# Kernel optimization log

Measured on AMD Instinct MI355X. Metric: run time of the kernel, lower is better.

## Reference

```python
import jax, jax.numpy as jnp
import numpy as np
from math import sqrt

B, S, E, H = 2, 2048, 768, 12
DH = E // H
W = 256            # one-sided attention window (attention_window=512)
G = 16             # number of global tokens (positions 0..G-1 in every batch row)
PAD = 128          # last PAD tokens per row are padding (masked)
FF = 3072          # SwiGLU intermediate size
NEG = -1e9
EPS = 1e-5


def _ln(x, g, b):
    m = jnp.mean(x, axis=-1, keepdims=True)
    v = jnp.var(x, axis=-1, keepdims=True)
    return (x - m) * jax.lax.rsqrt(v + EPS) * g + b


def _rope(x, t):
    # x: [B,H,S,DH]; t: [B,S] float 'set positions'
    half = DH // 2
    inv_freq = 1.0 / (10000.0 ** (jnp.arange(half, dtype=jnp.float32) / half))
    ang = t[:, None, :, None] * inv_freq            # [B,1,S,half]
    cos, sin = jnp.cos(ang), jnp.sin(ang)
    x1, x2 = x[..., :half], x[..., half:]
    return jnp.concatenate([x1 * cos - x2 * sin, x2 * cos + x1 * sin], axis=-1)


def _heads(x):  # [B,S,E] -> [B,H,S,DH]
    return x.reshape(B, S, H, DH).transpose(0, 2, 1, 3)


def _chunk3(x):
    # [B,H,S,D] -> [B,H,C,3W,D]: for query chunk c, keys from chunks c-1,c,c+1 (zero padded)
    b, h, s, d = x.shape
    c = s // W
    xp = jnp.pad(x, ((0, 0), (0, 0), (W, W), (0, 0))).reshape(b, h, c + 2, W, d)
    return jnp.concatenate([xp[:, :, :-2], xp[:, :, 1:-1], xp[:, :, 2:]], axis=3)


def _forward(x, attention_mask, global_attention_mask,
             Wq, bq, Wk, bk, Wv, bv, Wqg, bqg, Wkg, bkg, Wvg, bvg,
             ln0_g, ln0_b, ln1_g, ln1_b, W1, W3, W2):
    C = S // W
    merged = attention_mask * (global_attention_mask + 1)   # 0 masked, 1 local, 2 global
    is_masked = merged == 0
    is_global = merged == 2
    remove = merged != 1   # keys removed from windowed attention (masked or global)

    q = _heads(x @ Wq + bq) / sqrt(DH)
    k = _heads(x @ Wk + bk)
    v = _heads(x @ Wv + bv)

    # RoPE over 'set positions': (~is_index_masked) * cumsum(is_index_global_attn)
    t = jnp.where(is_masked, 0, jnp.cumsum(is_global.astype(jnp.int32), axis=1)).astype(jnp.float32)
    q = _rope(q, t)
    k = _rope(k, t)

    # --- sliding-window (banded) scores: band[b,h,i,d] = q_i . k_{i+d-W} ---
    qc = q.reshape(B, H, C, W, DH)
    k3 = _chunk3(k)
    s3 = jnp.einsum('bhcpd,bhcqd->bhcpq', qc, k3)                     # [B,H,C,W,3W]
    didx = jnp.arange(W)[:, None] + jnp.arange(2 * W + 1)[None, :]    # [W,2W+1]
    band = jnp.take_along_axis(s3, didx[None, None, None], axis=-1)   # [B,H,C,W,2W+1]

    # mask removed keys / out-of-range positions inside the band
    rmp = jnp.pad(remove, ((0, 0), (W, W)), constant_values=True).reshape(B, C + 2, W)
    rm3 = jnp.concatenate([rmp[:, :-2], rmp[:, 1:-1], rmp[:, 2:]], axis=2)  # [B,C,3W]
    band_rm = jnp.take_along_axis(jnp.broadcast_to(rm3[:, :, None, :], (B, C, W, 3 * W)),
                                  didx[None, None], axis=-1)                # [B,C,W,2W+1]
    band = jnp.where(band_rm[:, None], NEG, band).reshape(B, H, S, 2 * W + 1)

    # --- global-key columns (keys taken from the RoPE'd local key vectors) ---
    sg = jnp.einsum('bhid,bhgd->bhig', q, k[:, :, :G])                # [B,H,S,G]

    scores = jnp.concatenate([sg, band], axis=-1)                     # [B,H,S,G+2W+1]
    probs = jax.nn.softmax(scores.astype(jnp.float32), axis=-1).astype(x.dtype)
    probs = jnp.where(is_masked[:, None, :, None], 0.0, probs)

    # --- probs @ value: global columns + band ---
    out = jnp.einsum('bhig,bhgd->bhid', probs[..., :G], v[:, :, :G])
    pl = probs[..., G:].reshape(B, H, C, W, 2 * W + 1)
    rows = jnp.broadcast_to(jnp.arange(W)[:, None], (W, 2 * W + 1))
    p3 = jnp.zeros((B, H, C, W, 3 * W), probs.dtype).at[:, :, :, rows, didx].set(pl)
    v3 = _chunk3(v)
    out = out + jnp.einsum('bhcpq,bhcqd->bhcpd', p3, v3).reshape(B, H, S, DH)
    attn = out.transpose(0, 2, 1, 3).reshape(B, S, E)

    # --- full attention for global tokens (separate global projections, no RoPE) ---
    gq = _heads(x @ Wqg + bqg)[:, :, :G] / sqrt(DH)                   # [B,H,G,DH]
    gk = _heads(x @ Wkg + bkg)
    gv = _heads(x @ Wvg + bvg)
    gs = jnp.einsum('bhgd,bhjd->bhgj', gq, gk)                        # [B,H,G,S]
    gs = jnp.where(is_masked[:, None, None, :], NEG, gs)
    gp = jax.nn.softmax(gs.astype(jnp.float32), axis=-1).astype(x.dtype)
    gout = jnp.einsum('bhgj,bhjd->bhgd', gp, gv).transpose(0, 2, 1, 3).reshape(B, G, E)
    attn = attn.at[:, :G].set(gout)

    # residual + post-LN, SwiGLU FFN, residual + post-LN (dropout = eval mode)
    h0 = _ln(x + attn, ln0_g, ln0_b)
    ffn = (jax.nn.silu(h0 @ W1) * (h0 @ W3)) @ W2
    return _ln(h0 + ffn, ln1_g, ln1_b)


def setup_inputs():
    key = jax.random.key(0)
    ks = jax.random.split(key, 12)
    x = jax.random.normal(ks[0], (B, S, E), jnp.float32)
    attention_mask = jnp.ones((B, S), jnp.int32).at[:, S - PAD:].set(0)
    global_attention_mask = jnp.zeros((B, S), jnp.int32).at[:, :G].set(1)
    sd = 0.02
    def w(k, shape):
        return jax.random.normal(k, shape, jnp.float32) * sd
    return dict(
        x=x, attention_mask=attention_mask, global_attention_mask=global_attention_mask,
        Wq=w(ks[1], (E, E)), bq=jnp.zeros((E,), jnp.float32),
        Wk=w(ks[2], (E, E)), bk=jnp.zeros((E,), jnp.float32),
        Wv=w(ks[3], (E, E)), bv=jnp.zeros((E,), jnp.float32),
        Wqg=w(ks[4], (E, E)), bqg=jnp.zeros((E,), jnp.float32),
        Wkg=w(ks[5], (E, E)), bkg=jnp.zeros((E,), jnp.float32),
        Wvg=w(ks[6], (E, E)), bvg=jnp.zeros((E,), jnp.float32),
        ln0_g=jnp.ones((E,), jnp.float32), ln0_b=jnp.zeros((E,), jnp.float32),
        ln1_g=jnp.ones((E,), jnp.float32), ln1_b=jnp.zeros((E,), jnp.float32),
        W1=w(ks[7], (E, FF)), W3=w(ks[8], (E, FF)), W2=w(ks[9], (FF, E)))


def reference(x, attention_mask, global_attention_mask, Wq, bq, Wk, bk, Wv, bv,
              Wqg, bqg, Wkg, bkg, Wvg, bvg, ln0_g, ln0_b, ln1_g, ln1_b, W1, W3, W2):
    return _forward(x, attention_mask, global_attention_mask,
                    Wq, bq, Wk, bk, Wv, bv, Wqg, bqg, Wkg, bkg, Wvg, bvg,
                    ln0_g, ln0_b, ln1_g, ln1_b, W1, W3, W2)
```

## Files before the change

kernel.cpp:

```cpp
#include <hip/hip_runtime.h>


#define BB_ 2
#define SS 2048
#define EE 768
#define HH 12
#define DHH 64
#define GG 16
#define FFN 3072
#define MM (BB_*SS)

typedef __bf16 bf16_t;
typedef __bf16 bf16x8_t __attribute__((ext_vector_type(8)));
typedef float f32x4_t __attribute__((ext_vector_type(4)));

__device__ inline void gload16(const void* g, void* l) {
  __builtin_amdgcn_global_load_lds((const __attribute__((address_space(1))) void*)g,
                                   (__attribute__((address_space(3))) void*)l, 16, 0, 0);
}

__global__ __launch_bounds__(64) void detect_kernel(const unsigned int* __restrict__ w,
                                                    int* __restrict__ flag) {
  int cnt = 0;
  for (int i = threadIdx.x; i < 1024; i += 64) {
    unsigned e = (w[i] >> 7) & 0xFF;
    cnt += (e >= 100 && e <= 144) ? 1 : 0;
  }
  for (int off = 32; off; off >>= 1) cnt += __shfl_xor(cnt, off);
  if (threadIdx.x == 0) flag[0] = (cnt > 512) ? 1 : 0;
}

struct CanonP { const void* src[11]; bf16_t* dst[11]; };

__global__ __launch_bounds__(256) void canon_kernel(CanonP P, const int* __restrict__ flag) {
  constexpr int ns[11] = {3145728, 768,768,768,768,768,768, 768,768,768,768};
  int idx4 = (blockIdx.x*256 + threadIdx.x)*4;
  const bool isb = flag[0] != 0;
  int off = 0, seg = -1, loc = 0;
  #pragma unroll
  for (int i=0;i<11;i++) {
    if (seg < 0 && idx4 < off + ns[i]) { seg = i; loc = idx4 - off; }
    off += ns[i];
  }
  if (seg < 0) return;
  const void* s = P.src[seg];
  bf16_t* d = P.dst[seg];
  if (isb) {
    *(uint2*)&d[loc] = *(const uint2*)((const unsigned short*)s + loc);
  } else {
    float4 v = *(const float4*)((const float*)s + loc);
    d[loc+0] = (bf16_t)v.x; d[loc+1] = (bf16_t)v.y;
    d[loc+2] = (bf16_t)v.z; d[loc+3] = (bf16_t)v.w;
  }
}

struct TP6 { const void* s[6]; bf16_t* d[6]; };

__global__ __launch_bounds__(256) void trans_kernel(TP6 P, int R, int C,
                                                    const int* __restrict__ flag) {
  const int z = blockIdx.z;
  const void* src = P.s[z]; bf16_t* dst = P.d[z];
  const bool isb = flag[0] != 0;
  __shared__ bf16_t tile[32][33];
  int tx = threadIdx.x & 31, ty = threadIdx.x >> 5;
  int r0 = blockIdx.y*32, c0 = blockIdx.x*32;
  #pragma unroll
  for (int i=0;i<4;i++) {
    int rr = ty + i*8;
    size_t si = (size_t)(r0+rr)*C + c0 + tx;
    tile[rr][tx] = isb ? ((const bf16_t*)src)[si] : (bf16_t)((const float*)src)[si];
  }
  __syncthreads();
  #pragma unroll
  for (int i=0;i<4;i++) {
    int cc = ty + i*8;
    dst[(size_t)(c0+cc)*R + r0 + tx] = tile[tx][cc];
  }
}

__global__ __launch_bounds__(256) void zero_kernel(float* __restrict__ p, int n) {
  int i = blockIdx.x*256 + threadIdx.x;
  if (i < n) p[i] = 0.f;
}

__global__ __launch_bounds__(256) void flags_kernel(const int* __restrict__ am,
                                                    const int* __restrict__ gm,
                                                    float* __restrict__ tpos,
                                                    int* __restrict__ flags) {
  int b = blockIdx.x;
  int t = threadIdx.x;
  int lane = t & 63, wv = t >> 6;
  int base = b*SS + t*8;
  int mg[8]; int isg[8]; int loc = 0;
  for (int i=0;i<8;i++) {
    int a = am[base+i], g = gm[base+i];
    int merged = a*(g+1);
    mg[i] = merged;
    isg[i] = (merged==2) ? 1 : 0;
    loc += isg[i];
  }
  int x = loc;
  for (int off=1; off<64; off<<=1) {
    int y = __shfl_up(x, off);
    if (lane >= off) x += y;
  }
  __shared__ int wtot[4];
  if (lane==63) wtot[wv] = x;
  __syncthreads();
  int prev = 0;
  for (int w=0; w<wv; w++) prev += wtot[w];
  int run = prev + x - loc;
  for (int i=0;i<8;i++) {
    run += isg[i];
    int masked = (mg[i]==0) ? 1 : 0;
    int glob   = (mg[i]==2) ? 1 : 0;
    int rem    = (mg[i]!=1) ? 1 : 0;
    tpos[base+i]  = masked ? 0.f : (float)run;
    flags[base+i] = masked | (glob<<1) | (rem<<2);
  }
}

__device__ inline void gemm128_core(const bf16_t* __restrict__ A,
                                    const bf16_t* __restrict__ BT,
                                    int ldA, int ldB, int kbeg, int kend,
                                    int m0, int n0,
                                    bf16_t* As, bf16_t* Bs,
                                    f32x4_t (&acc)[4][4]) {
  const int t = threadIdx.x;
  const int lane = t & 63, wv = t >> 6;
  const int l15 = lane & 15, quad = lane >> 4;
  const int wr = (wv >> 1) << 6, wc = (wv & 1) << 6;
  const int rsub = lane >> 3, pch = lane & 7;
  const int sch = pch ^ rsub;
  const size_t abase = (size_t)(m0 + wv*32 + rsub)*ldA + sch*8;
  const size_t bbase = (size_t)(n0 + wv*32 + rsub)*ldB + sch*8;
  const int sx = l15 & 7;
  bf16_t* lA = As + (wv*32)*64;
  bf16_t* lB = Bs + (wv*32)*64;
  for (int k0 = kbeg; k0 < kend; k0 += 64) {
    __syncthreads();
    #pragma unroll
    for (int j=0;j<4;j++) {
      gload16(A + abase + (size_t)(j*8)*ldA + k0, lA + j*8*64);
      gload16(BT + bbase + (size_t)(j*8)*ldB + k0, lB + j*8*64);
    }
    __syncthreads();
    #pragma unroll
    for (int c=0;c<2;c++) {
      bf16x8_t af[4], bfr[4];
      #pragma unroll
      for (int a=0;a<4;a++)
        af[a] = *(const bf16x8_t*)&As[(wr + a*16 + l15)*64 + ((c*4+quad)^sx)*8];
      #pragma unroll
      for (int b=0;b<4;b++)
        bfr[b] = *(const bf16x8_t*)&Bs[(wc + b*16 + l15)*64 + ((c*4+quad)^sx)*8];
      #pragma unroll
      for (int a=0;a<4;a++)
        #pragma unroll
        for (int b=0;b<4;b++)
          acc[a][b] = __builtin_amdgcn_mfma_f32_16x16x32_bf16(af[a], bfr[b], acc[a][b], 0,0,0);
    }
  }
}

struct ProjParams {
  const bf16_t* W[5];
  const bf16_t* Bi[5];
  bf16_t* O[5];
};

__global__ __launch_bounds__(256) void proj_kernel(const bf16_t* __restrict__ x,
                                                   ProjParams P,
                                                   const float* __restrict__ tpos) {
  const int m0 = blockIdx.x*128, n0 = blockIdx.y*128;
  const int z  = blockIdx.z;
  __shared__ bf16_t As[128*64];
  __shared__ bf16_t Bs[128*64];
  f32x4_t acc[4][4];
  #pragma unroll
  for (int a=0;a<4;a++)
    #pragma unroll
    for (int b=0;b<4;b++) acc[a][b] = (f32x4_t){0.f,0.f,0.f,0.f};
  gemm128_core(x, P.W[z], EE, EE, 0, EE, m0, n0, As, Bs, acc);

  const int t = threadIdx.x;
  const int lane = t & 63, wv = t >> 6;
  const int l15 = lane & 15, quad = lane >> 4;
  const int wr = (wv >> 1) << 6, wc = (wv & 1) << 6;
  const float scale = (z==0) ? 0.125f : 1.f;
  const bool rope = (z<2);
  const int h = (n0 + wc) >> 6;
  bf16_t* Oz = P.O[z];
  const bf16_t* Bz = P.Bi[z];
  float bvals[4];
  #pragma unroll
  for (int b=0;b<4;b++) bvals[b] = (float)Bz[h*64 + b*16 + l15];
  #pragma unroll
  for (int a=0;a<4;a++) {
    #pragma unroll
    for (int r=0;r<4;r++) {
      int row = m0 + wr + a*16 + quad*4 + r;
      int bb = row >> 11, spos = row & (SS-1);
      float vals[4];
      #pragma unroll
      for (int b=0;b<4;b++) vals[b] = (acc[a][b][r] + bvals[b]) * scale;
      if (rope) {
        float tv = tpos[row];
        #pragma unroll
        for (int b=0;b<2;b++) {
          int j = b*16 + l15;
          float inv = __expf(-(float)j * (9.210340371976184f/32.f));
          float ang = tv * inv;
          float sn = __sinf(ang), cs = __cosf(ang);
          float x1 = vals[b], x2 = vals[b+2];
          vals[b]   = x1*cs - x2*sn;
          vals[b+2] = x2*cs + x1*sn;
        }
      }
      bf16_t* dst = Oz + ((size_t)(bb*HH + h)*SS + spos)*DHH;
      #pragma unroll
      for (int b=0;b<4;b++) dst[b*16 + l15] = (bf16_t)vals[b];
    }
  }
}

__global__ __launch_bounds__(256) void gemm_ffn13(const bf16_t* __restrict__ A,
                                                  const bf16_t* __restrict__ B1T,
                                                  const bf16_t* __restrict__ B3T,
                                                  bf16_t* __restrict__ g1) {
  const int m0 = blockIdx.x*128, n0 = blockIdx.y*128;
  const int t = threadIdx.x;
  const int lane = t & 63, wv = t >> 6;
  const int l15 = lane & 15, quad = lane >> 4;
  const int wr = (wv >> 1) << 6, wc = (wv & 1) << 6;
  const int rsub = lane >> 3, pch = lane & 7;
  const int sch = pch ^ rsub;
  const int sx = l15 & 7;
  __shared__ bf16_t As[128*64];
  __shared__ bf16_t B1s[128*64];
  __shared__ bf16_t B3s[128*64];
  f32x4_t acc1[4][4], acc3[4][4];
  #pragma unroll
  for (int a=0;a<4;a++)
    #pragma unroll
    for (int b=0;b<4;b++) {
      acc1[a][b] = (f32x4_t){0.f,0.f,0.f,0.f};
      acc3[a][b] = (f32x4_t){0.f,0.f,0.f,0.f};
    }
  const size_t abase = (size_t)(m0 + wv*32 + rsub)*EE + sch*8;
  const size_t bbase = (size_t)(n0 + wv*32 + rsub)*EE + sch*8;
  bf16_t* lA  = As  + (wv*32)*64;
  bf16_t* lB1 = B1s + (wv*32)*64;
  bf16_t* lB3 = B3s + (wv*32)*64;
  for (int k0 = 0; k0 < EE; k0 += 64) {
    __syncthreads();
    #pragma unroll
    for (int j=0;j<4;j++) {
      gload16(A   + abase + (size_t)(j*8)*EE + k0, lA  + j*8*64);
      gload16(B1T + bbase + (size_t)(j*8)*EE + k0, lB1 + j*8*64);
      gload16(B3T + bbase + (size_t)(j*8)*EE + k0, lB3 + j*8*64);
    }
    __syncthreads();
    #pragma unroll
    for (int c=0;c<2;c++) {
      bf16x8_t af[4], b1f[4], b3f[4];
      #pragma unroll
      for (int a=0;a<4;a++)
        af[a] = *(const bf16x8_t*)&As[(wr + a*16 + l15)*64 + ((c*4+quad)^sx)*8];
      #pragma unroll
      for (int b=0;b<4;b++) {
        b1f[b] = *(const bf16x8_t*)&B1s[(wc + b*16 + l15)*64 + ((c*4+quad)^sx)*8];
        b3f[b] = *(const bf16x8_t*)&B3s[(wc + b*16 + l15)*64 + ((c*4+quad)^sx)*8];
      }
      #pragma unroll
      for (int a=0;a<4;a++)
        #pragma unroll
        for (int b=0;b<4;b++) {
          acc1[a][b] = __builtin_amdgcn_mfma_f32_16x16x32_bf16(af[a], b1f[b], acc1[a][b], 0,0,0);
          acc3[a][b] = __builtin_amdgcn_mfma_f32_16x16x32_bf16(af[a], b3f[b], acc3[a][b], 0,0,0);
        }
    }
  }
  #pragma unroll
  for (int a=0;a<4;a++)
    #pragma unroll
    for (int r=0;r<4;r++) {
      int row = m0 + wr + a*16 + quad*4 + r;
      #pragma unroll
      for (int b=0;b<4;b++) {
        float a1 = acc1[a][b][r];
        float sil = a1 / (1.f + __expf(-a1));
        g1[(size_t)row*FFN + n0 + wc + b*16 + l15] = (bf16_t)(sil * acc3[a][b][r]);
      }
    }
}

struct Ffn2Out { float* p[4]; };

__global__ __launch_bounds__(256) void gemm_ffn2(const bf16_t* __restrict__ A,
                                                 const bf16_t* __restrict__ BT,
                                                 Ffn2Out O) {
  const int m0 = blockIdx.x*128, n0 = blockIdx.y*128;
  const int kz = blockIdx.z;
  __shared__ bf16_t As[128*64];
  __shared__ bf16_t Bs[128*64];
  f32x4_t acc[4][4];
  #pragma unroll
  for (int a=0;a<4;a++)
    #pragma unroll
    for (int b=0;b<4;b++) acc[a][b] = (f32x4_t){0.f,0.f,0.f,0.f};
  gemm128_core(A, BT, FFN, FFN, kz*768, (kz+1)*768, m0, n0, As, Bs, acc);
  const int t = threadIdx.x;
  const int lane = t & 63, wv = t >> 6;
  const int l15 = lane & 15, quad = lane >> 4;
  const int wr = (wv >> 1) << 6, wc = (wv & 1) << 6;
  float* C = O.p[kz];
  #pragma unroll
  for (int a=0;a<4;a++)
    #pragma unroll
    for (int r=0;r<4;r++) {
      int row = m0 + wr + a*16 + quad*4 + r;
      #pragma unroll
      for (int b=0;b<4;b++)
        C[(size_t)row*EE + n0 + wc + b*16 + l15] = acc[a][b][r];
    }
}

__global__ __launch_bounds__(64) void qg_kernel(const bf16_t* __restrict__ x,
                                                const bf16_t* __restrict__ WqgT,
                                                const bf16_t* __restrict__ bqg,
                                                float* __restrict__ qgb) {
  int g = blockIdx.x, h = blockIdx.y, b = blockIdx.z;
  int d = threadIdx.x;
  __shared__ float xs[EE];
  for (int i=d; i<EE; i+=64) xs[i] = (float)x[((size_t)b*SS + g)*EE + i];
  __syncthreads();
  float acc = 0.f;
  const bf16_t* wrow = WqgT + (size_t)(h*64+d)*EE;
  for (int k=0;k<EE;k++) acc += xs[k] * (float)wrow[k];
  acc = (acc + (float)bqg[h*64+d]) * 0.125f;
  qgb[((size_t)(b*HH+h)*GG + g)*DHH + d] = acc;
}

__global__ __launch_bounds__(256) void band_kernel(const bf16_t* __restrict__ qb,
                                                   const bf16_t* __restrict__ kb,
                                                   const bf16_t* __restrict__ vb,
                                                   const int* __restrict__ flags,
                                                   float* __restrict__ attn) {
  const int p0 = blockIdx.x*64;
  const int h = blockIdx.y, b = blockIdx.z;
  const int t = threadIdx.x;
  const int wv = t>>6, lane = t&63;
  const int l15 = lane & 15, quad = lane >> 4;
  const size_t bh = (size_t)(b*HH+h);
  const bf16_t* kbh = kb + bh*SS*DHH;
  const bf16_t* vbh = vb + bh*SS*DHH;
  const int* fl = flags + b*SS;
  const int q0 = p0 + wv*16;

  __shared__ bf16_t Vt[64*72];
  __shared__ bf16_t Pw[4][16*72];

  const bf16_t* qrow = qb + (bh*SS + q0 + l15)*DHH;
  bf16x8_t qa0 = *(const bf16x8_t*)(qrow + quad*8);
  bf16x8_t qa1 = *(const bf16x8_t*)(qrow + 32 + quad*8);

  f32x4_t o[4];
  #pragma unroll
  for (int i=0;i<4;i++) o[i] = (f32x4_t){0.f,0.f,0.f,0.f};
  float lsum[4] = {0.f,0.f,0.f,0.f};
  bf16_t* P = Pw[wv];

  for (int unit=0; unit<10; unit++) {
    const int kb0 = (unit<9) ? (p0 - 256 + unit*64) : 0;
    __syncthreads();
    {
      int kp  = (t & 31)*2;
      int dh0 = (t >> 5)*8;
      int k1 = kb0 + kp, k2 = kb0 + kp + 1;
      int kc1 = min(max(k1,0),SS-1), kc2 = min(max(k2,0),SS-1);
      bf16x8_t v1 = *(const bf16x8_t*)(vbh + (size_t)kc1*DHH + dh0);
      bf16x8_t v2 = *(const bf16x8_t*)(vbh + (size_t)kc2*DHH + dh0);
      #pragma unroll
      for (int i=0;i<8;i++) {
        union { unsigned u; bf16_t hh[2]; } pk;
        pk.hh[0] = v1[i]; pk.hh[1] = v2[i];
        *(unsigned*)&Vt[(dh0+i)*72 + kp] = pk.u;
      }
    }
    __syncthreads();
    const int nsub = (unit<9) ? 4 : 1;
    for (int sub=0; sub<4; sub++) {
      if (sub < nsub) {
        int kpos = kb0 + sub*16 + l15;
        int kc = min(max(kpos,0),SS-1);
        const bf16_t* krow = kbh + (size_t)kc*DHH;
        bf16x8_t kf0 = *(const bf16x8_t*)(krow + quad*8);
        bf16x8_t kf1 = *(const bf16x8_t*)(krow + 32 + quad*8);
        f32x4_t s = (f32x4_t){0.f,0.f,0.f,0.f};
        s = __builtin_amdgcn_mfma_f32_16x16x32_bf16(qa0, kf0, s, 0,0,0);
        s = __builtin_amdgcn_mfma_f32_16x16x32_bf16(qa1, kf1, s, 0,0,0);
        bool drop = false;
        if (unit<9) drop = (kpos<0) || (kpos>=SS) || (((fl[kc]>>2)&1)!=0);
        #pragma unroll
        for (int r=0;r<4;r++) {
          float e;
          if (unit==9) {
            e = __expf(s[r]);
          } else {
            int dj = kpos - (q0 + quad*4 + r);
            bool valid = (dj>=-256) && (dj<=256) && (!drop);
            e = valid ? __expf(s[r]) : 0.f;
          }
          lsum[r] += e;
          P[(quad*4+r)*72 + sub*16 + l15] = (bf16_t)e;
        }
      } else {
        #pragma unroll
        for (int r=0;r<4;r++) P[(quad*4+r)*72 + sub*16 + l15] = (bf16_t)0.f;
      }
    }
    #pragma unroll
    for (int chunk=0; chunk<2; chunk++) {
      bf16x8_t pf = *(const bf16x8_t*)&P[l15*72 + chunk*32 + quad*8];
      #pragma unroll
      for (int nt=0; nt<4; nt++) {
        bf16x8_t vf = *(const bf16x8_t*)&Vt[(nt*16+l15)*72 + chunk*32 + quad*8];
        o[nt] = __builtin_amdgcn_mfma_f32_16x16x32_bf16(pf, vf, o[nt], 0,0,0);
      }
    }
  }
  #pragma unroll
  for (int r=0;r<4;r++) {
    float s = lsum[r];
    s += __shfl_xor(s,1); s += __shfl_xor(s,2);
    s += __shfl_xor(s,4); s += __shfl_xor(s,8);
    lsum[r] = s;
  }
  #pragma unroll
  for (int r=0;r<4;r++) {
    int q = q0 + quad*4 + r;
    int masked = fl[q] & 1;
    float inv = masked ? 0.f : 1.f/lsum[r];
    float* dst = attn + ((size_t)(b*SS+q))*EE + h*64 + l15;
    #pragma unroll
    for (int nt=0; nt<4; nt++) dst[nt*16] = o[nt][r]*inv;
  }
}

__global__ __launch_bounds__(256) void gattn_part(const float* __restrict__ qgb,
                                                  const bf16_t* __restrict__ kgb,
                                                  const bf16_t* __restrict__ vgb,
                                                  const int* __restrict__ flags,
                                                  float* __restrict__ go,
                                                  float* __restrict__ gl) {
  const int kbase = blockIdx.x*128;
  const int h = blockIdx.y, b = blockIdx.z;
  const int t = threadIdx.x;
  __shared__ float gqs[16*68];
  __shared__ float Ks[64*68];
  __shared__ float Vs[64*68];
  __shared__ float es[16*64];
  const size_t bh = (size_t)(b*HH+h);
  #pragma unroll
  for (int j=0;j<4;j++) {
    int idx = t + j*256;
    int g = idx>>6, d = idx&63;
    gqs[g*68+d] = qgb[(bh*GG + g)*DHH + d];
  }
  float accv[4] = {0.f,0.f,0.f,0.f};
  float lpart = 0.f;
  const int gs = t>>4, kslot = t&15;
  const int dp = t&63, grp = t>>6;
  const bf16_t* kb_ = kgb + bh*SS*DHH;
  const bf16_t* vb_ = vgb + bh*SS*DHH;
  const int* fl = flags + b*SS;
  for (int tile=0; tile<2; tile++) {
    int k0 = kbase + tile*64;
    __syncthreads();
    {
      int row = t>>2, seg = t&3;
      const bf16_t* sk = kb_ + (size_t)(k0+row)*DHH + seg*16;
      const bf16_t* sv = vb_ + (size_t)(k0+row)*DHH + seg*16;
      bf16x8_t k1 = *(const bf16x8_t*)sk;
      bf16x8_t k2 = *(const bf16x8_t*)(sk+8);
      bf16x8_t v1 = *(const bf16x8_t*)sv;
      bf16x8_t v2 = *(const bf16x8_t*)(sv+8);
      #pragma unroll
      for (int i=0;i<8;i++) {
        Ks[row*68 + seg*16 + i]     = (float)k1[i];
        Ks[row*68 + seg*16 + 8 + i] = (float)k2[i];
        Vs[row*68 + seg*16 + i]     = (float)v1[i];
        Vs[row*68 + seg*16 + 8 + i] = (float)v2[i];
      }
    }
    __syncthreads();
    #pragma unroll
    for (int j=0;j<4;j++) {
      int key = kslot + 16*j;
      const float* gq = &gqs[gs*68];
      const float* kr = &Ks[key*68];
      float s = 0.f;
      #pragma unroll
      for (int d4=0; d4<64; d4+=4) {
        float4 a = *(const float4*)(gq + d4);
        float4 kk = *(const float4*)(kr + d4);
        s += a.x*kk.x + a.y*kk.y + a.z*kk.z + a.w*kk.w;
      }
      int msk = fl[k0+key] & 1;
      float e = msk ? 0.f : __expf(s);
      es[gs*64+key] = e;
      lpart += e;
    }
    __syncthreads();
    #pragma unroll
    for (int g=0; g<4; g++) {
      int gg = grp*4+g;
      float a = accv[g];
      for (int key=0;key<64;key++) a += es[gg*64+key]*Vs[key*68+dp];
      accv[g] = a;
    }
  }
  __syncthreads();
  es[gs*64 + kslot] = lpart;
  __syncthreads();
  if (t < 16) {
    float s = 0.f;
    for (int j=0;j<16;j++) s += es[t*64+j];
    atomicAdd(&gl[bh*16 + t], s);
  }
  #pragma unroll
  for (int g=0; g<4; g++)
    atomicAdd(&go[(bh*16 + grp*4+g)*64 + dp], accv[g]);
}

__global__ __launch_bounds__(256) void gattn_fin(const float* __restrict__ go,
                                                 const float* __restrict__ gl,
                                                 float* __restrict__ attn) {
  int idx = blockIdx.x*256 + threadIdx.x;
  int dp = idx & 63;
  int g  = (idx >> 6) & 15;
  int h  = (idx >> 10) % HH;
  int b  = idx / (1024*HH);
  attn[((size_t)b*SS + g)*EE + h*64 + dp] = go[idx] / gl[idx>>6];
}

__global__ __launch_bounds__(256) void addln_kernel(const bf16_t* __restrict__ Abf,
                                                    const float* __restrict__ Af,
                                                    const float* __restrict__ B0,
                                                    const float* __restrict__ B1,
                                                    const float* __restrict__ B2,
                                                    const float* __restrict__ B3,
                                                    const bf16_t* __restrict__ gw,
                                                    const bf16_t* __restrict__ bw,
                                                    float* __restrict__ outf,
                                                    bf16_t* __restrict__ outb,
                                                    const int* __restrict__ flagp) {
  int r = blockIdx.x, t = threadIdx.x;
  int lane = t&63, wv = t>>6;
  float v[3]; float sum=0.f, ss=0.f;
  #pragma unroll
  for (int j=0;j<3;j++) {
    int idx = t + j*256;
    size_t gi = (size_t)r*EE+idx;
    float a = Abf ? (float)Abf[gi] : Af[gi];
    float val = a + B0[gi];
    if (B1) val += B1[gi] + B2[gi] + B3[gi];
    v[j] = val; sum += val; ss += val*val;
  }
  #pragma unroll
  for (int off=32; off>=1; off>>=1) {
    sum += __shfl_xor(sum, off);
    ss  += __shfl_xor(ss, off);
  }
  __shared__ float s1[4], s2[4];
  if (lane==0) { s1[wv]=sum; s2[wv]=ss; }
  __syncthreads();
  sum = s1[0]+s1[1]+s1[2]+s1[3];
  ss  = s2[0]+s2[1]+s2[2]+s2[3];
  float mean = sum * (1.f/(float)EE);
  float var  = ss * (1.f/(float)EE) - mean*mean;
  float rstd = rsqrtf(var + 1e-5f);
  bool wantb, wantf;
  if (flagp) { bool isb = (*flagp)!=0; wantb = isb; wantf = !isb; }
  else { wantb = (outb!=nullptr); wantf = (outf!=nullptr); }
  #pragma unroll
  for (int j=0;j<3;j++) {
    int idx = t + j*256;
    float o = (v[j]-mean)*rstd*(float)gw[idx] + (float)bw[idx];
    if (wantf) outf[(size_t)r*EE+idx] = o;
    if (wantb) outb[(size_t)r*EE+idx] = (bf16_t)o;
  }
}

extern "C" void kernel_launch(void* const* d_in, const int* in_sizes, int n_in,
                              void* d_out, int out_size, void* d_ws, size_t ws_size,
                              hipStream_t stream) {
  const void* x_r    = d_in[0];
  const int* am      = (const int*)d_in[1];
  const int* gm      = (const int*)d_in[2];
  (void)in_sizes; (void)n_in; (void)out_size; (void)ws_size;

  char* ws = (char*)d_ws;
  size_t off = 0;
  auto alloc = [&](size_t bytes) -> void* {
    void* p = ws + off;
    off += (bytes + 255) & ~(size_t)255;
    return p;
  };
  bf16_t* xc    = (bf16_t*)alloc((size_t)MM*EE*2);
  bf16_t* WT[6]; bf16_t* bc[6];
  for (int i=0;i<6;i++) { WT[i] = (bf16_t*)alloc((size_t)EE*EE*2); bc[i] = (bf16_t*)alloc(EE*2); }
  bf16_t* lnc[4];
  for (int i=0;i<4;i++) lnc[i] = (bf16_t*)alloc(EE*2);
  bf16_t* W1T = (bf16_t*)alloc((size_t)EE*FFN*2);
  bf16_t* W3T = (bf16_t*)alloc((size_t)EE*FFN*2);
  bf16_t* W2T = (bf16_t*)alloc((size_t)FFN*EE*2);
  const size_t NBHSD = (size_t)BB_*HH*SS*DHH;
  bf16_t* qb    = (bf16_t*)alloc(NBHSD*2);
  bf16_t* kb    = (bf16_t*)alloc(NBHSD*2);
  bf16_t* vb    = (bf16_t*)alloc(NBHSD*2);
  bf16_t* kgb   = (bf16_t*)alloc(NBHSD*2);
  bf16_t* vgb   = (bf16_t*)alloc(NBHSD*2);
  float* qgb   = (float*)alloc((size_t)BB_*HH*GG*DHH*4);
  float* attn  = (float*)alloc((size_t)MM*EE*4);
  float* h0f   = (float*)alloc((size_t)MM*EE*4);
  bf16_t* h0b  = (bf16_t*)alloc((size_t)MM*EE*2);
  bf16_t* g1   = (bf16_t*)alloc((size_t)MM*FFN*2);
  float* p3    = (float*)alloc((size_t)MM*EE*4);
  float* go    = (float*)alloc((size_t)BB_*HH*GG*DHH*4);
  float* gl    = (float*)alloc((size_t)BB_*HH*GG*4);
  float* tposb = (float*)alloc((size_t)BB_*SS*4);
  int*   flagb = (int*)alloc((size_t)BB_*SS*4);
  int*   dflag = (int*)alloc(256);
  float* p1 = (float*)qb;
  float* p2 = (float*)qb + (size_t)MM*EE;

  detect_kernel<<<1, 64, 0, stream>>>((const unsigned int*)d_in[3], dflag);

  CanonP CP;
  const void* csrc[11] = { x_r, d_in[4], d_in[6], d_in[8], d_in[10], d_in[12], d_in[14],
                           d_in[15], d_in[16], d_in[17], d_in[18] };
  bf16_t* cdst[11] = { xc, bc[0], bc[1], bc[2], bc[3], bc[4], bc[5],
                       lnc[0], lnc[1], lnc[2], lnc[3] };
  for (int i=0;i<11;i++) { CP.src[i]=csrc[i]; CP.dst[i]=cdst[i]; }
  canon_kernel<<<3081, 256, 0, stream>>>(CP, dflag);

  TP6 T6;
  const int wi[6] = {3,5,7,9,11,13};
  for (int i=0;i<6;i++) { T6.s[i]=d_in[wi[i]]; T6.d[i]=WT[i]; }
  trans_kernel<<<dim3(24,24,6), 256, 0, stream>>>(T6, EE, EE, dflag);
  TP6 TF; TF.s[0]=d_in[19]; TF.d[0]=W1T; TF.s[1]=d_in[20]; TF.d[1]=W3T;
  for (int i=2;i<6;i++) { TF.s[i]=d_in[19]; TF.d[i]=W1T; }
  trans_kernel<<<dim3(96,24,2), 256, 0, stream>>>(TF, EE, FFN, dflag);
  TP6 T2; T2.s[0]=d_in[21]; T2.d[0]=W2T;
  for (int i=1;i<6;i++) { T2.s[i]=d_in[21]; T2.d[i]=W2T; }
  trans_kernel<<<dim3(24,96,1), 256, 0, stream>>>(T2, FFN, EE, dflag);

  zero_kernel<<<98, 256, 0, stream>>>(go, 24960);

  flags_kernel<<<BB_, 256, 0, stream>>>(am, gm, tposb, flagb);

  ProjParams P;
  P.W[0]=WT[0]; P.Bi[0]=bc[0]; P.O[0]=qb;
  P.W[1]=WT[1]; P.Bi[1]=bc[1]; P.O[1]=kb;
  P.W[2]=WT[2]; P.Bi[2]=bc[2]; P.O[2]=vb;
  P.W[3]=WT[4]; P.Bi[3]=bc[4]; P.O[3]=kgb;
  P.W[4]=WT[5]; P.Bi[4]=bc[5]; P.O[4]=vgb;
  proj_kernel<<<dim3(MM/128, EE/128, 5), 256, 0, stream>>>(xc, P, tposb);

  qg_kernel<<<dim3(GG, HH, BB_), 64, 0, stream>>>(xc, WT[3], bc[3], qgb);

  band_kernel<<<dim3(SS/64, HH, BB_), 256, 0, stream>>>(qb, kb, vb, flagb, attn);

  gattn_part<<<dim3(SS/128, HH, BB_), 256, 0, stream>>>(qgb, kgb, vgb, flagb, go, gl);
  gattn_fin<<<96, 256, 0, stream>>>(go, gl, attn);

  addln_kernel<<<MM, 256, 0, stream>>>(xc, nullptr, attn, nullptr, nullptr, nullptr,
                                       lnc[0], lnc[1], h0f, h0b, nullptr);

  gemm_ffn13<<<dim3(MM/128, FFN/128), 256, 0, stream>>>(h0b, W1T, W3T, g1);
  Ffn2Out FO; FO.p[0]=attn; FO.p[1]=p1; FO.p[2]=p2; FO.p[3]=p3;
  gemm_ffn2<<<dim3(MM/128, EE/128, 4), 256, 0, stream>>>(g1, W2T, FO);

  addln_kernel<<<MM, 256, 0, stream>>>(nullptr, h0f, attn, p1, p2, p3,
                                       lnc[2], lnc[3],
                                       (float*)d_out, (bf16_t*)d_out, dflag);
}
```

Baseline: 398.4 us.

## Split fused FFN1/FFN3 GEMM, fold global-attn finalize into LayerNorm, vectorize qg

Splits the dual-accumulator W1/W3 GEMM into two single-weight GEMMs that share the common gemm128_core. The first writes the W1 product to a bf16 scratch buffer, and the second applies SiLU-gating in its epilogue. This halves accumulator registers and LDS per block to improve occupancy, at the cost of an extra pass over A and a bf16 intermediate round-trip that also rounds the gate input. The global-attention normalize kernel is removed and its division is folded into the first add+LayerNorm, and the qg projection loop now reads weights as 8-wide bf16 vectors.

```diff
diff --git a/kernel.cpp b/kernel.cpp
--- a/kernel.cpp
+++ b/kernel.cpp
@@ -224,73 +224,61 @@
   }
 }
 
-__global__ __launch_bounds__(256) void gemm_ffn13(const bf16_t* __restrict__ A,
-                                                  const bf16_t* __restrict__ B1T,
-                                                  const bf16_t* __restrict__ B3T,
-                                                  bf16_t* __restrict__ g1) {
+__global__ __launch_bounds__(256) void gemm_ffn1(const bf16_t* __restrict__ A,
+                                                 const bf16_t* __restrict__ BT,
+                                                 bf16_t* __restrict__ t1) {
   const int m0 = blockIdx.x*128, n0 = blockIdx.y*128;
+  __shared__ bf16_t As[128*64];
+  __shared__ bf16_t Bs[128*64];
+  f32x4_t acc[4][4];
+  #pragma unroll
+  for (int a=0;a<4;a++)
+    #pragma unroll
+    for (int b=0;b<4;b++) acc[a][b] = (f32x4_t){0.f,0.f,0.f,0.f};
+  gemm128_core(A, BT, EE, EE, 0, EE, m0, n0, As, Bs, acc);
   const int t = threadIdx.x;
   const int lane = t & 63, wv = t >> 6;
   const int l15 = lane & 15, quad = lane >> 4;
   const int wr = (wv >> 1) << 6, wc = (wv & 1) << 6;
-  const int rsub = lane >> 3, pch = lane & 7;
-  const int sch = pch ^ rsub;
-  const int sx = l15 & 7;
-  __shared__ bf16_t As[128*64];
-  __shared__ bf16_t B1s[128*64];
-  __shared__ bf16_t B3s[128*64];
-  f32x4_t acc1[4][4], acc3[4][4];
-  #pragma unroll
-  for (int a=0;a<4;a++)
-    #pragma unroll
-    for (int b=0;b<4;b++) {
-      acc1[a][b] = (f32x4_t){0.f,0.f,0.f,0.f};
-      acc3[a][b] = (f32x4_t){0.f,0.f,0.f,0.f};
-    }
-  const size_t abase = (size_t)(m0 + wv*32 + rsub)*EE + sch*8;
-  const size_t bbase = (size_t)(n0 + wv*32 + rsub)*EE + sch*8;
-  bf16_t* lA  = As  + (wv*32)*64;
-  bf16_t* lB1 = B1s + (wv*32)*64;
-  bf16_t* lB3 = B3s + (wv*32)*64;
-  for (int k0 = 0; k0 < EE; k0 += 64) {
-    __syncthreads();
-    #pragma unroll
-    for (int j=0;j<4;j++) {
-      gload16(A   + abase + (size_t)(j*8)*EE + k0, lA  + j*8*64);
-      gload16(B1T + bbase + (size_t)(j*8)*EE + k0, lB1 + j*8*64);
-      gload16(B3T + bbase + (size_t)(j*8)*EE + k0, lB3 + j*8*64);
-    }
-    __syncthreads();
-    #pragma unroll
-    for (int c=0;c<2;c++) {
-      bf16x8_t af[4], b1f[4], b3f[4];
-      #pragma unroll
-      for (int a=0;a<4;a++)
-        af[a] = *(const bf16x8_t*)&As[(wr + a*16 + l15)*64 + ((c*4+quad)^sx)*8];
-      #pragma unroll
-      for (int b=0;b<4;b++) {
-        b1f[b] = *(const bf16x8_t*)&B1s[(wc + b*16 + l15)*64 + ((c*4+quad)^sx)*8];
-        b3f[b] = *(const bf16x8_t*)&B3s[(wc + b*16 + l15)*64 + ((c*4+quad)^sx)*8];
-      }
-      #pragma unroll
-      for (int a=0;a<4;a++)
-        #pragma unroll
-        for (int b=0;b<4;b++) {
-          acc1[a][b] = __builtin_amdgcn_mfma_f32_16x16x32_bf16(af[a], b1f[b], acc1[a][b], 0,0,0);
-          acc3[a][b] = __builtin_amdgcn_mfma_f32_16x16x32_bf16(af[a], b3f[b], acc3[a][b], 0,0,0);
-        }
-    }
-  }
   #pragma unroll
   for (int a=0;a<4;a++)
     #pragma unroll
     for (int r=0;r<4;r++) {
       int row = m0 + wr + a*16 + quad*4 + r;
       #pragma unroll
+      for (int b=0;b<4;b++)
+        t1[(size_t)row*FFN + n0 + wc + b*16 + l15] = (bf16_t)acc[a][b][r];
+    }
+}
+
+__global__ __launch_bounds__(256) void gemm_ffn3(const bf16_t* __restrict__ A,
+                                                 const bf16_t* __restrict__ BT,
+                                                 const bf16_t* __restrict__ t1,
+                                                 bf16_t* __restrict__ g1) {
+  const int m0 = blockIdx.x*128, n0 = blockIdx.y*128;
+  __shared__ bf16_t As[128*64];
+  __shared__ bf16_t Bs[128*64];
+  f32x4_t acc[4][4];
+  #pragma unroll
+  for (int a=0;a<4;a++)
+    #pragma unroll
+    for (int b=0;b<4;b++) acc[a][b] = (f32x4_t){0.f,0.f,0.f,0.f};
+  gemm128_core(A, BT, EE, EE, 0, EE, m0, n0, As, Bs, acc);
+  const int t = threadIdx.x;
+  const int lane = t & 63, wv = t >> 6;
+  const int l15 = lane & 15, quad = lane >> 4;
+  const int wr = (wv >> 1) << 6, wc = (wv & 1) << 6;
+  #pragma unroll
+  for (int a=0;a<4;a++)
+    #pragma unroll
+    for (int r=0;r<4;r++) {
+      int row = m0 + wr + a*16 + quad*4 + r;
+      #pragma unroll
       for (int b=0;b<4;b++) {
-        float a1 = acc1[a][b][r];
+        size_t idx = (size_t)row*FFN + n0 + wc + b*16 + l15;
+        float a1 = (float)t1[idx];
         float sil = a1 / (1.f + __expf(-a1));
-        g1[(size_t)row*FFN + n0 + wc + b*16 + l15] = (bf16_t)(sil * acc3[a][b][r]);
+        g1[idx] = (bf16_t)(sil * acc[a][b][r]);
       }
     }
 }
@@ -337,7 +325,12 @@
   __syncthreads();
   float acc = 0.f;
   const bf16_t* wrow = WqgT + (size_t)(h*64+d)*EE;
-  for (int k=0;k<EE;k++) acc += xs[k] * (float)wrow[k];
+  #pragma unroll 4
+  for (int k=0;k<EE;k+=8) {
+    bf16x8_t w8 = *(const bf16x8_t*)(wrow + k);
+    #pragma unroll
+    for (int i=0;i<8;i++) acc += xs[k+i] * (float)w8[i];
+  }
   acc = (acc + (float)bqg[h*64+d]) * 0.125f;
   qgb[((size_t)(b*HH+h)*GG + g)*DHH + d] = acc;
 }
@@ -534,23 +527,14 @@
     atomicAdd(&go[(bh*16 + grp*4+g)*64 + dp], accv[g]);
 }
 
-__global__ __launch_bounds__(256) void gattn_fin(const float* __restrict__ go,
-                                                 const float* __restrict__ gl,
-                                                 float* __restrict__ attn) {
-  int idx = blockIdx.x*256 + threadIdx.x;
-  int dp = idx & 63;
-  int g  = (idx >> 6) & 15;
-  int h  = (idx >> 10) % HH;
-  int b  = idx / (1024*HH);
-  attn[((size_t)b*SS + g)*EE + h*64 + dp] = go[idx] / gl[idx>>6];
-}
-
 __global__ __launch_bounds__(256) void addln_kernel(const bf16_t* __restrict__ Abf,
                                                     const float* __restrict__ Af,
                                                     const float* __restrict__ B0,
                                                     const float* __restrict__ B1,
                                                     const float* __restrict__ B2,
                                                     const float* __restrict__ B3,
+                                                    const float* __restrict__ gof,
+                                                    const float* __restrict__ glf,
                                                     const bf16_t* __restrict__ gw,
                                                     const bf16_t* __restrict__ bw,
                                                     float* __restrict__ outf,
@@ -558,13 +542,23 @@
                                                     const int* __restrict__ flagp) {
   int r = blockIdx.x, t = threadIdx.x;
   int lane = t&63, wv = t>>6;
+  int spos = r & (SS-1), bb = r >> 11;
+  bool isglob = (gof != nullptr) && (spos < GG);
   float v[3]; float sum=0.f, ss=0.f;
   #pragma unroll
   for (int j=0;j<3;j++) {
     int idx = t + j*256;
     size_t gi = (size_t)r*EE+idx;
     float a = Abf ? (float)Abf[gi] : Af[gi];
-    float val = a + B0[gi];
+    float bv;
+    if (isglob) {
+      int hh = idx >> 6, dp = idx & 63;
+      int slot = (bb*HH + hh)*GG + spos;
+      bv = gof[(size_t)slot*DHH + dp] / glf[slot];
+    } else {
+      bv = B0[gi];
+    }
+    float val = a + bv;
     if (B1) val += B1[gi] + B2[gi] + B3[gi];
     v[j] = val; sum += val; ss += val*val;
   }
@@ -633,6 +627,7 @@
   float* tposb = (float*)alloc((size_t)BB_*SS*4);
   int*   flagb = (int*)alloc((size_t)BB_*SS*4);
   int*   dflag = (int*)alloc(256);
+  bf16_t* t1 = qb;
   float* p1 = (float*)qb;
   float* p2 = (float*)qb + (size_t)MM*EE;
 
@@ -674,16 +669,16 @@
   band_kernel<<<dim3(SS/64, HH, BB_), 256, 0, stream>>>(qb, kb, vb, flagb, attn);
 
   gattn_part<<<dim3(SS/128, HH, BB_), 256, 0, stream>>>(qgb, kgb, vgb, flagb, go, gl);
-  gattn_fin<<<96, 256, 0, stream>>>(go, gl, attn);
 
   addln_kernel<<<MM, 256, 0, stream>>>(xc, nullptr, attn, nullptr, nullptr, nullptr,
-                                       lnc[0], lnc[1], h0f, h0b, nullptr);
-
-  gemm_ffn13<<<dim3(MM/128, FFN/128), 256, 0, stream>>>(h0b, W1T, W3T, g1);
+                                       go, gl, lnc[0], lnc[1], h0f, h0b, nullptr);
+
+  gemm_ffn1<<<dim3(MM/128, FFN/128), 256, 0, stream>>>(h0b, W1T, t1);
+  gemm_ffn3<<<dim3(MM/128, FFN/128), 256, 0, stream>>>(h0b, W3T, t1, g1);
   Ffn2Out FO; FO.p[0]=attn; FO.p[1]=p1; FO.p[2]=p2; FO.p[3]=p3;
   gemm_ffn2<<<dim3(MM/128, EE/128, 4), 256, 0, stream>>>(g1, W2T, FO);
 
   addln_kernel<<<MM, 256, 0, stream>>>(nullptr, h0f, attn, p1, p2, p3,
-                                       lnc[2], lnc[3],
+                                       nullptr, nullptr, lnc[2], lnc[3],
                                        (float*)d_out, (bf16_t*)d_out, dflag);
 }
```

Result: no change. 392.3 us (-1.5%).
